# Performance work log

Hardware: AMD Instinct MI355X
Metric: run time of the kernel (lower is better)

The kernel has to match this reference:

```python
import jax, jax.numpy as jnp
import numpy as np

N = 50000   # n_nodes
E = 500000  # n_edges
D = 128     # input_dim == hidden_dim
L = 2       # n_layers
K = 5       # Chebyshev filter size


def setup_inputs() -> dict:
    key = jax.random.key(0)
    k0, k1, k2, k3, k4 = jax.random.split(key, 5)
    scale = 1.0 / np.sqrt(D)
    return {
        "edge_index": jax.random.randint(k0, (2, E), 0, N),
        "edge_weight": jax.random.uniform(k1, (E,), dtype=jnp.float32),
        "emb": jax.random.uniform(k2, (N, D), dtype=jnp.float32, minval=-1.0, maxval=1.0),
        "Wx": jax.random.normal(k3, (L, 3, K, D, D), dtype=jnp.float32) * scale,
        "bx": jnp.zeros((L, 3, D), dtype=jnp.float32),
        "Wh": jax.random.normal(k4, (L, 3, K, D, D), dtype=jnp.float32) * scale,
        "bh": jnp.zeros((L, 3, D), dtype=jnp.float32),
    }


def reference(edge_index, edge_weight, emb, Wx, bx, Wh, bh):
    src, dst = edge_index[0], edge_index[1]
    # ChebConv sym-normalized scaled Laplacian with lambda_max=2:
    # L_hat = L - I = -D^{-1/2} A D^{-1/2} (zero diagonal)
    deg = jax.ops.segment_sum(edge_weight, src, num_segments=N)
    dinv = jnp.where(deg > 0, deg ** -0.5, 0.0)
    w = -dinv[src] * edge_weight * dinv[dst]  # [E]

    def prop(x):  # L_hat @ x via gather/scatter over edges
        return jax.ops.segment_sum(w[:, None] * x[src], dst, num_segments=N)

    def cheb(x, W, b):  # sum_k T_k(L_hat) x W_k + b
        Tx0 = x
        out = Tx0 @ W[0]
        Tx1 = prop(Tx0)
        out = out + Tx1 @ W[1]
        for k in range(2, K):
            Tx2 = 2.0 * prop(Tx1) - Tx0
            out = out + Tx2 @ W[k]
            Tx0, Tx1 = Tx1, Tx2
        return out + b

    x = emb
    hidden_states = []
    for l in range(L):
        H = jnp.ones((N, D), x.dtype)  # init__hidd: ones
        Z = jax.nn.sigmoid(cheb(x, Wx[l, 0], bx[l, 0]) + cheb(H, Wh[l, 0], bh[l, 0]))
        R = jax.nn.sigmoid(cheb(x, Wx[l, 1], bx[l, 1]) + cheb(H, Wh[l, 1], bh[l, 1]))
        Ht = jnp.tanh(cheb(x, Wx[l, 2], bx[l, 2]) + cheb(H * R, Wh[l, 2], bh[l, 2]))
        Hn = Z * H + (1.0 - Z) * Ht
        h = jax.nn.relu(Hn)  # dropout is identity in eval mode
        hidden_states.append(h)
        x = h
    return x  # == hidden_states[-1]
```

## Files before the change

kernel.cpp:

```cpp
#include <hip/hip_runtime.h>
#include <math.h>

#define NN 50000
#define EE 500000
#define DD 128
#define KK 5
#define LL 2

typedef _Float16 f16x8 __attribute__((ext_vector_type(8)));
typedef float f32x4 __attribute__((ext_vector_type(4)));

__device__ __forceinline__ ushort f2h(float x) {
    union { _Float16 h; ushort u; } v; v.h = (_Float16)x; return v.u;
}


__global__ __launch_bounds__(256) void edge_pass1(
    const int* __restrict__ src, const int* __restrict__ dst,
    const float* __restrict__ ew,
    float* __restrict__ deg, int* __restrict__ hist)
{
    int e = blockIdx.x * blockDim.x + threadIdx.x;
    if (e >= EE) return;
    atomicAdd(&deg[src[e]], ew[e]);
    atomicAdd(&hist[dst[e]], 1);
}

__global__ __launch_bounds__(256) void dinv_kernel(
    const float* __restrict__ deg, float* __restrict__ dinv)
{
    int i = blockIdx.x * blockDim.x + threadIdx.x;
    if (i >= NN) return;
    float d = deg[i];
    dinv[i] = (d > 0.f) ? (1.f / sqrtf(d)) : 0.f;
}

#define SCAN_C ((NN + 1023) / 1024)
__global__ __launch_bounds__(1024) void scan_kernel(
    const int* __restrict__ hist, int* __restrict__ row_ptr)
{
    __shared__ int sums[1024];
    const int t = threadIdx.x;
    const int base = t * SCAN_C;
    int local[SCAN_C];
    int s = 0;
#pragma unroll
    for (int j = 0; j < SCAN_C; ++j) {
        int i = base + j;
        int v = (i < NN) ? hist[i] : 0;
        s += v;
        local[j] = s;
    }
    sums[t] = s;
    __syncthreads();
    for (int off = 1; off < 1024; off <<= 1) {
        int v = (t >= off) ? sums[t - off] : 0;
        __syncthreads();
        sums[t] += v;
        __syncthreads();
    }
    int excl = sums[t] - s;
    if (t == 0) row_ptr[0] = 0;
#pragma unroll
    for (int j = 0; j < SCAN_C; ++j) {
        int i = base + j;
        if (i < NN) row_ptr[i + 1] = excl + local[j];
    }
}

__global__ __launch_bounds__(256) void copy_fill(
    const int* __restrict__ row_ptr, int* __restrict__ fill)
{
    int i = blockIdx.x * blockDim.x + threadIdx.x;
    if (i < NN) fill[i] = row_ptr[i];
}

__global__ __launch_bounds__(256) void edge_scatter(
    const int* __restrict__ src, const int* __restrict__ dst,
    const float* __restrict__ ew, const float* __restrict__ dinv,
    int* __restrict__ fill,
    int* __restrict__ src_srt, float* __restrict__ w_srt)
{
    int e = blockIdx.x * blockDim.x + threadIdx.x;
    if (e >= EE) return;
    int s = src[e], t = dst[e];
    float w = -dinv[s] * ew[e] * dinv[t];
    int pos = atomicAdd(&fill[t], 1);
    src_srt[pos] = s;
    w_srt[pos] = w;
}

__global__ __launch_bounds__(256) void propv_kernel(
    const int* __restrict__ rp, const int* __restrict__ ss, const float* __restrict__ sw,
    const float* __restrict__ tin, const float* __restrict__ tprev, float* __restrict__ tout,
    float alpha, float beta, int ones_in, int ones_prev)
{
    int i = blockIdx.x * blockDim.x + threadIdx.x;
    if (i >= NN) return;
    float acc = 0.f;
    int e0 = rp[i], e1 = rp[i + 1];
    int e = e0;
    for (; e + 4 <= e1; e += 4) {
        float t0 = ones_in ? 1.f : tin[ss[e]];
        float t1v = ones_in ? 1.f : tin[ss[e + 1]];
        float t2v = ones_in ? 1.f : tin[ss[e + 2]];
        float t3v = ones_in ? 1.f : tin[ss[e + 3]];
        acc += sw[e] * t0 + sw[e + 1] * t1v + sw[e + 2] * t2v + sw[e + 3] * t3v;
    }
    for (; e < e1; ++e) {
        float tv = ones_in ? 1.f : tin[ss[e]];
        acc += sw[e] * tv;
    }
    float pv = ones_prev ? 1.f : (tprev ? tprev[i] : 0.f);
    tout[i] = alpha * acc + beta * pv;
}

__global__ __launch_bounds__(128) void colsum_kernel(
    const float* __restrict__ Wh, float* __restrict__ scol)
{
    int b = blockIdx.x;
    int k = b % KK;
    int g = (b / KK) % 2;
    int l = b / (2 * KK);
    int d = threadIdx.x;
    const float* Wp = Wh + ((size_t)((l * 3 + g) * KK + k)) * DD * DD;
    float s = 0.f;
    for (int r = 0; r < DD; ++r) s += Wp[r * DD + d];
    scol[((size_t)((l * 2 + g) * KK + k)) * DD + d] = s;
}

__global__ __launch_bounds__(256) void wconv_f16(
    const float* __restrict__ W, ushort* __restrict__ out, int mode)
{
    int t = blockIdx.x;
    int st = (mode == 0) ? t : ((t / KK) * 3 + 2) * KK + (t % KK);
    const float* Wp = W + (size_t)st * DD * DD;
    ushort* op = out + (size_t)t * DD * DD;
    for (int idx = threadIdx.x; idx < DD * DD; idx += 256) {
        int rb = idx >> 7, c = idx & 127;
        float w = Wp[c * DD + rb];
        int byte = rb * 256 + (((c * 2) ^ ((rb & 7) << 4)));
        *(ushort*)((char*)op + byte) = f2h(w);
    }
}

__global__ __launch_bounds__(256) void f32_to_f16(
    const float* __restrict__ in, ushort* __restrict__ out, int n8)
{
    int i = blockIdx.x * blockDim.x + threadIdx.x;
    if (i >= n8) return;
    float4 a = ((const float4*)in)[i * 2];
    float4 b = ((const float4*)in)[i * 2 + 1];
    f16x8 o;
    o[0] = (_Float16)a.x; o[1] = (_Float16)a.y; o[2] = (_Float16)a.z; o[3] = (_Float16)a.w;
    o[4] = (_Float16)b.x; o[5] = (_Float16)b.y; o[6] = (_Float16)b.z; o[7] = (_Float16)b.w;
    ((f16x8*)out)[i] = o;
}

__global__ __launch_bounds__(256) void prop_mat(
    const int* __restrict__ rp, const int* __restrict__ ss, const float* __restrict__ sw,
    const ushort* __restrict__ x, const ushort* __restrict__ prev,
    ushort* __restrict__ out, float alpha, float beta)
{
    int node = blockIdx.x * 16 + (threadIdx.x >> 4);
    if (node >= NN) return;
    int lane = threadIdx.x & 15;
    int c = lane * 8;
    float acc[8];
#pragma unroll
    for (int j = 0; j < 8; ++j) acc[j] = 0.f;
    int e0 = rp[node], e1 = rp[node + 1];
    int e = e0;
    for (; e + 4 <= e1; e += 4) {
        int s0 = ss[e], s1 = ss[e + 1], s2 = ss[e + 2], s3 = ss[e + 3];
        float w0 = sw[e], w1 = sw[e + 1], w2 = sw[e + 2], w3 = sw[e + 3];
        f16x8 r0 = *(const f16x8*)(x + (size_t)s0 * DD + c);
        f16x8 r1 = *(const f16x8*)(x + (size_t)s1 * DD + c);
        f16x8 r2 = *(const f16x8*)(x + (size_t)s2 * DD + c);
        f16x8 r3 = *(const f16x8*)(x + (size_t)s3 * DD + c);
#pragma unroll
        for (int j = 0; j < 8; ++j)
            acc[j] += w0 * (float)r0[j] + w1 * (float)r1[j] + w2 * (float)r2[j] + w3 * (float)r3[j];
    }
    for (; e < e1; ++e) {
        int s = ss[e];
        float w = sw[e];
        f16x8 r = *(const f16x8*)(x + (size_t)s * DD + c);
#pragma unroll
        for (int j = 0; j < 8; ++j) acc[j] += w * (float)r[j];
    }
    f16x8 o;
    if (beta != 0.f && prev) {
        f16x8 pv = *(const f16x8*)(prev + (size_t)node * DD + c);
#pragma unroll
        for (int j = 0; j < 8; ++j) o[j] = (_Float16)(alpha * acc[j] + beta * (float)pv[j]);
    } else {
#pragma unroll
        for (int j = 0; j < 8; ++j) o[j] = (_Float16)(alpha * acc[j]);
    }
    *(f16x8*)(out + (size_t)node * DD + c) = o;
}

__device__ __forceinline__ void mm_gate(
    const ushort* __restrict__ const* Ts, const ushort* __restrict__ Wg,
    ushort* Bs, int rowg0, int rowg1, bool ok0, bool ok1,
    int tid, int lk, f32x4 acc[2][8], int lr)
{
#pragma unroll
    for (int fr = 0; fr < 2; ++fr)
#pragma unroll
        for (int fc = 0; fc < 8; ++fc) acc[fr][fc] = (f32x4){0.f, 0.f, 0.f, 0.f};
#pragma unroll
    for (int k = 0; k < KK; ++k) {
        const ushort* Tk = Ts[k];
        const ushort* Bg = Wg + (size_t)k * (DD * DD);
        __syncthreads();
#pragma unroll
        for (int i = 0; i < 8; ++i) {
            int off = i * 4096 + tid * 16;
            uint4 v = *(const uint4*)((const char*)Bg + off);
            *(uint4*)((char*)Bs + off) = v;
        }
        f16x8 a[2][4];
#pragma unroll
        for (int fr = 0; fr < 2; ++fr) {
            int rowg = fr ? rowg1 : rowg0;
            bool ok = fr ? ok1 : ok0;
            const ushort* rp2 = Ts[k] + (size_t)rowg * DD + lk * 8;
            (void)Tk;
#pragma unroll
            for (int ko = 0; ko < 4; ++ko) {
                if (ok) a[fr][ko] = *(const f16x8*)(rp2 + ko * 32);
                else a[fr][ko] = (f16x8){0, 0, 0, 0, 0, 0, 0, 0};
            }
        }
        __syncthreads();
#pragma unroll
        for (int ko = 0; ko < 4; ++ko) {
            const int cb = ko * 64 + lk * 16;
#pragma unroll
            for (int fc = 0; fc < 8; ++fc) {
                int rb = fc * 16 + lr;
                int byte = (rb * 256 + cb) ^ ((rb & 7) << 4);
                f16x8 bfrag = *(const f16x8*)((const char*)Bs + byte);
                acc[0][fc] = __builtin_amdgcn_mfma_f32_16x16x32_f16(a[0][ko], bfrag, acc[0][fc], 0, 0, 0);
                acc[1][fc] = __builtin_amdgcn_mfma_f32_16x16x32_f16(a[1][ko], bfrag, acc[1][fc], 0, 0, 0);
            }
        }
    }
}

__device__ __forceinline__ int xcd_swz(int b, int nwg) {
    int xcd = b & 7, idx = b >> 3;
    int q = nwg >> 3, rr = nwg & 7;
    int start = (xcd < rr) ? xcd * (q + 1) : rr * (q + 1) + (xcd - rr) * q;
    return start + idx;
}

__global__ __launch_bounds__(256) void cheb_mm_zr(
    const ushort* __restrict__ T0, const ushort* __restrict__ T1,
    const ushort* __restrict__ T2, const ushort* __restrict__ T3,
    const ushort* __restrict__ T4,
    const ushort* __restrict__ Wt,
    const float* __restrict__ tvec, const float* __restrict__ scol,
    const float* __restrict__ bx, const float* __restrict__ bh, int l,
    float* __restrict__ Xz, ushort* __restrict__ Xr16, float* __restrict__ Xh)
{
    __shared__ ushort Bs[DD * DD];
    const int tile = xcd_swz(blockIdx.x, gridDim.x);
    const int tid = threadIdx.x;
    const int lane = tid & 63;
    const int wid = tid >> 6;
    const int lr = lane & 15;
    const int lk = lane >> 4;
    const int r0 = tile * 128;
    const ushort* Ts[5] = {T0, T1, T2, T3, T4};

    int rowg0 = r0 + wid * 32 + lr;
    int rowg1 = rowg0 + 16;
    bool ok0 = rowg0 < NN;
    bool ok1 = rowg1 < NN;

    f32x4 accZ[2][8], accB[2][8];
    mm_gate(Ts, Wt, Bs, rowg0, rowg1, ok0, ok1, tid, lk, accZ, lr);
    mm_gate(Ts, Wt + (size_t)KK * DD * DD, Bs, rowg0, rowg1, ok0, ok1, tid, lk, accB, lr);

    {
        const float* s0 = scol + (size_t)((l * 2 + 0) * KK) * DD;
        const float* s1 = scol + (size_t)((l * 2 + 1) * KK) * DD;
        const float* bz0 = bx + (size_t)(l * 3 + 0) * DD;
        const float* bz1 = bh + (size_t)(l * 3 + 0) * DD;
        const float* br0 = bx + (size_t)(l * 3 + 1) * DD;
        const float* br1 = bh + (size_t)(l * 3 + 1) * DD;
#pragma unroll
        for (int fr = 0; fr < 2; ++fr) {
#pragma unroll
            for (int j = 0; j < 4; ++j) {
                int grow = r0 + wid * 32 + fr * 16 + lk * 4 + j;
                if (grow < NN) {
                    float t1 = tvec[grow], t2 = tvec[NN + grow];
                    float t3 = tvec[2 * NN + grow], t4 = tvec[3 * NN + grow];
#pragma unroll
                    for (int fc = 0; fc < 8; ++fc) {
                        int d = fc * 16 + lr;
                        size_t idx = (size_t)grow * DD + d;
                        float hz = s0[d] + t1 * s0[DD + d] + t2 * s0[2 * DD + d]
                                 + t3 * s0[3 * DD + d] + t4 * s0[4 * DD + d];
                        float z = accZ[fr][fc][j] + bz0[d] + bz1[d] + hz;
                        z = 1.f / (1.f + expf(-z));
                        float hr = s1[d] + t1 * s1[DD + d] + t2 * s1[2 * DD + d]
                                 + t3 * s1[3 * DD + d] + t4 * s1[4 * DD + d];
                        float r = accB[fr][fc][j] + br0[d] + br1[d] + hr;
                        r = 1.f / (1.f + expf(-r));
                        Xz[idx] = z;
                        Xr16[idx] = f2h(r);
                    }
                }
            }
        }
    }

    mm_gate(Ts, Wt + (size_t)2 * KK * DD * DD, Bs, rowg0, rowg1, ok0, ok1, tid, lk, accZ, lr);
#pragma unroll
    for (int fr = 0; fr < 2; ++fr) {
#pragma unroll
        for (int j = 0; j < 4; ++j) {
            int grow = r0 + wid * 32 + fr * 16 + lk * 4 + j;
            if (grow < NN) {
#pragma unroll
                for (int fc = 0; fc < 8; ++fc) {
                    int d = fc * 16 + lr;
                    Xh[(size_t)grow * DD + d] = accZ[fr][fc][j];
                }
            }
        }
    }
}

__global__ __launch_bounds__(256) void cheb_mm_final(
    const ushort* __restrict__ T0, const ushort* __restrict__ T1,
    const ushort* __restrict__ T2, const ushort* __restrict__ T3,
    const ushort* __restrict__ T4,
    const ushort* __restrict__ Wt,
    const float* __restrict__ Xh, const float* __restrict__ Xz,
    const float* __restrict__ bx, const float* __restrict__ bh, int l,
    float* __restrict__ out, ushort* __restrict__ h16, int write_f32)
{
    __shared__ ushort Bs[DD * DD];
    const int tile = xcd_swz(blockIdx.x, gridDim.x);
    const int tid = threadIdx.x;
    const int lane = tid & 63;
    const int wid = tid >> 6;
    const int lr = lane & 15;
    const int lk = lane >> 4;
    const int r0 = tile * 128;
    const ushort* Ts[5] = {T0, T1, T2, T3, T4};

    int rowg0 = r0 + wid * 32 + lr;
    int rowg1 = rowg0 + 16;
    bool ok0 = rowg0 < NN;
    bool ok1 = rowg1 < NN;

    f32x4 acc[2][8];
    mm_gate(Ts, Wt, Bs, rowg0, rowg1, ok0, ok1, tid, lk, acc, lr);

    const float* b0 = bx + (size_t)(l * 3 + 2) * DD;
    const float* b1 = bh + (size_t)(l * 3 + 2) * DD;
#pragma unroll
    for (int fr = 0; fr < 2; ++fr) {
#pragma unroll
        for (int j = 0; j < 4; ++j) {
            int grow = r0 + wid * 32 + fr * 16 + lk * 4 + j;
            if (grow < NN) {
#pragma unroll
                for (int fc = 0; fc < 8; ++fc) {
                    int d = fc * 16 + lr;
                    size_t idx = (size_t)grow * DD + d;
                    float pre = acc[fr][fc][j] + Xh[idx] + b0[d] + b1[d];
                    float ht = tanhf(pre);
                    float z = Xz[idx];
                    float hn = z + (1.f - z) * ht;
                    float h = hn > 0.f ? hn : 0.f;
                    if (write_f32) out[idx] = h;
                    h16[idx] = f2h(h);
                }
            }
        }
    }
}


extern "C" void kernel_launch(void* const* d_in, const int* in_sizes, int n_in,
                              void* d_out, int out_size, void* d_ws, size_t ws_size,
                              hipStream_t stream)
{
    const int*   ei  = (const int*)d_in[0];
    const float* ew  = (const float*)d_in[1];
    const float* emb = (const float*)d_in[2];
    const float* Wx  = (const float*)d_in[3];
    const float* bx  = (const float*)d_in[4];
    const float* Wh  = (const float*)d_in[5];
    const float* bh  = (const float*)d_in[6];
    float* out = (float*)d_out;

    const int* src = ei;
    const int* dst = ei + EE;

    char* ws = (char*)d_ws;
    size_t off = 0;
    auto alloc = [&](size_t nbytes) -> char* {
        char* p = ws + off;
        off = (off + nbytes + 255) & ~(size_t)255;
        return p;
    };
    float*  deg     = (float*)alloc((size_t)NN * 4);
    float*  dinv    = (float*)alloc((size_t)NN * 4);
    int*    hist    = (int*)alloc((size_t)(NN + 1) * 4);
    int*    row_ptr = (int*)alloc((size_t)(NN + 1) * 4);
    int*    fill    = (int*)alloc((size_t)(NN + 1) * 4);
    int*    src_srt = (int*)alloc((size_t)EE * 4);
    float*  w_srt   = (float*)alloc((size_t)EE * 4);
    float*  tvec    = (float*)alloc((size_t)4 * NN * 4);
    float*  scol    = (float*)alloc((size_t)LL * 2 * KK * DD * 4);
    float*  Xz      = (float*)alloc((size_t)NN * DD * 4);
    float*  Xh      = (float*)alloc((size_t)NN * DD * 4);
    ushort* Th      = (ushort*)alloc((size_t)4 * NN * DD * 2);
    ushort* x_f16   = (ushort*)alloc((size_t)NN * DD * 2);
    ushort* Xr_f16  = (ushort*)alloc((size_t)NN * DD * 2);
    ushort* WxT     = (ushort*)alloc((size_t)LL * 3 * KK * DD * DD * 2);
    ushort* WhT2    = (ushort*)alloc((size_t)LL * KK * DD * DD * 2);
    (void)ws_size; (void)in_sizes; (void)n_in; (void)out_size;

    ushort* T1 = Th;
    ushort* T2 = Th + (size_t)NN * DD;
    ushort* T3 = Th + (size_t)2 * NN * DD;
    ushort* T4 = Th + (size_t)3 * NN * DD;

    const int EG = (EE + 255) / 256;
    const int NG = (NN + 255) / 256;
    const int PG = (NN + 15) / 16;
    const int MMG = (NN + 127) / 128;
    const int CVG = (NN * DD / 8 + 255) / 256;
    const int GATE_STRIDE = KK * DD * DD;

    hipMemsetAsync(deg, 0, (size_t)NN * 4, stream);
    hipMemsetAsync(hist, 0, (size_t)(NN + 1) * 4, stream);

    edge_pass1<<<EG, 256, 0, stream>>>(src, dst, ew, deg, hist);
    dinv_kernel<<<NG, 256, 0, stream>>>(deg, dinv);
    scan_kernel<<<1, 1024, 0, stream>>>(hist, row_ptr);
    copy_fill<<<NG, 256, 0, stream>>>(row_ptr, fill);
    edge_scatter<<<EG, 256, 0, stream>>>(src, dst, ew, dinv, fill, src_srt, w_srt);

    float* t1 = tvec;
    float* t2 = tvec + NN;
    float* t3 = tvec + 2 * NN;
    float* t4 = tvec + 3 * NN;
    propv_kernel<<<NG, 256, 0, stream>>>(row_ptr, src_srt, w_srt, nullptr, nullptr, t1, 1.f,  0.f, 1, 0);
    propv_kernel<<<NG, 256, 0, stream>>>(row_ptr, src_srt, w_srt, t1, nullptr,      t2, 2.f, -1.f, 0, 1);
    propv_kernel<<<NG, 256, 0, stream>>>(row_ptr, src_srt, w_srt, t2, t1,           t3, 2.f, -1.f, 0, 0);
    propv_kernel<<<NG, 256, 0, stream>>>(row_ptr, src_srt, w_srt, t3, t2,           t4, 2.f, -1.f, 0, 0);

    colsum_kernel<<<LL * 2 * KK, 128, 0, stream>>>(Wh, scol);

    wconv_f16<<<LL * 3 * KK, 256, 0, stream>>>(Wx, WxT, 0);
    wconv_f16<<<LL * KK, 256, 0, stream>>>(Wh, WhT2, 1);

    f32_to_f16<<<CVG, 256, 0, stream>>>(emb, x_f16, NN * DD / 8);

    for (int l = 0; l < LL; ++l) {
        prop_mat<<<PG, 256, 0, stream>>>(row_ptr, src_srt, w_srt, x_f16, nullptr, T1, 1.f,  0.f);
        prop_mat<<<PG, 256, 0, stream>>>(row_ptr, src_srt, w_srt, T1,    x_f16,   T2, 2.f, -1.f);
        prop_mat<<<PG, 256, 0, stream>>>(row_ptr, src_srt, w_srt, T2,    T1,      T3, 2.f, -1.f);
        prop_mat<<<PG, 256, 0, stream>>>(row_ptr, src_srt, w_srt, T3,    T2,      T4, 2.f, -1.f);

        cheb_mm_zr<<<MMG, 256, 0, stream>>>(x_f16, T1, T2, T3, T4,
                                            WxT + (size_t)l * 3 * GATE_STRIDE,
                                            tvec, scol, bx, bh, l,
                                            Xz, Xr_f16, Xh);

        prop_mat<<<PG, 256, 0, stream>>>(row_ptr, src_srt, w_srt, Xr_f16, nullptr, T1, 1.f,  0.f);
        prop_mat<<<PG, 256, 0, stream>>>(row_ptr, src_srt, w_srt, T1,     Xr_f16,  T2, 2.f, -1.f);
        prop_mat<<<PG, 256, 0, stream>>>(row_ptr, src_srt, w_srt, T2,     T1,      T3, 2.f, -1.f);
        prop_mat<<<PG, 256, 0, stream>>>(row_ptr, src_srt, w_srt, T3,     T2,      T4, 2.f, -1.f);

        cheb_mm_final<<<MMG, 256, 0, stream>>>(Xr_f16, T1, T2, T3, T4,
                                               WhT2 + (size_t)l * GATE_STRIDE,
                                               Xh, Xz, bx, bh, l,
                                               out, x_f16, (l == LL - 1) ? 1 : 0);
    }
}
```

Measured before the change: 957.5 us.

## Split gate matmuls across blocks and unroll SpMM edge loop by eight

The fused x-side Chebyshev matmul kernel, which computed all three gates sequentially per 128-row tile, is replaced by a generic kernel launched with three times as many blocks, one gate each. This writes raw fp32 gate outputs to a new buffer, and a separate elementwise kernel applies the sigmoid for Z and R. The aim is more parallelism and fewer live accumulators per block. The cost is an extra fp32 write and read of the R pre-activation plus a new kernel launch. Separately, the sparse propagation loop gains an 8-edge unrolled path to put more gathers in flight.

```diff
diff --git a/kernel.cpp b/kernel.cpp
--- a/kernel.cpp
+++ b/kernel.cpp
@@ -171,6 +171,24 @@
     for (int j = 0; j < 8; ++j) acc[j] = 0.f;
     int e0 = rp[node], e1 = rp[node + 1];
     int e = e0;
+    for (; e + 8 <= e1; e += 8) {
+        int s0 = ss[e], s1 = ss[e + 1], s2 = ss[e + 2], s3 = ss[e + 3];
+        int s4 = ss[e + 4], s5 = ss[e + 5], s6 = ss[e + 6], s7 = ss[e + 7];
+        float w0 = sw[e], w1 = sw[e + 1], w2 = sw[e + 2], w3 = sw[e + 3];
+        float w4 = sw[e + 4], w5 = sw[e + 5], w6 = sw[e + 6], w7 = sw[e + 7];
+        f16x8 r0 = *(const f16x8*)(x + (size_t)s0 * DD + c);
+        f16x8 r1 = *(const f16x8*)(x + (size_t)s1 * DD + c);
+        f16x8 r2 = *(const f16x8*)(x + (size_t)s2 * DD + c);
+        f16x8 r3 = *(const f16x8*)(x + (size_t)s3 * DD + c);
+        f16x8 r4 = *(const f16x8*)(x + (size_t)s4 * DD + c);
+        f16x8 r5 = *(const f16x8*)(x + (size_t)s5 * DD + c);
+        f16x8 r6 = *(const f16x8*)(x + (size_t)s6 * DD + c);
+        f16x8 r7 = *(const f16x8*)(x + (size_t)s7 * DD + c);
+#pragma unroll
+        for (int j = 0; j < 8; ++j)
+            acc[j] += w0 * (float)r0[j] + w1 * (float)r1[j] + w2 * (float)r2[j] + w3 * (float)r3[j]
+                    + w4 * (float)r4[j] + w5 * (float)r5[j] + w6 * (float)r6[j] + w7 * (float)r7[j];
+    }
     for (; e + 4 <= e1; e += 4) {
         int s0 = ss[e], s1 = ss[e + 1], s2 = ss[e + 2], s3 = ss[e + 3];
         float w0 = sw[e], w1 = sw[e + 1], w2 = sw[e + 2], w3 = sw[e + 3];
@@ -212,7 +230,6 @@
         for (int fc = 0; fc < 8; ++fc) acc[fr][fc] = (f32x4){0.f, 0.f, 0.f, 0.f};
 #pragma unroll
     for (int k = 0; k < KK; ++k) {
-        const ushort* Tk = Ts[k];
         const ushort* Bg = Wg + (size_t)k * (DD * DD);
         __syncthreads();
 #pragma unroll
@@ -227,7 +244,6 @@
             int rowg = fr ? rowg1 : rowg0;
             bool ok = fr ? ok1 : ok0;
             const ushort* rp2 = Ts[k] + (size_t)rowg * DD + lk * 8;
-            (void)Tk;
 #pragma unroll
             for (int ko = 0; ko < 4; ++ko) {
                 if (ok) a[fr][ko] = *(const f16x8*)(rp2 + ko * 32);
@@ -257,17 +273,18 @@
     return start + idx;
 }
 
-__global__ __launch_bounds__(256) void cheb_mm_zr(
+__global__ __launch_bounds__(256) void cheb_mm_mfma(
     const ushort* __restrict__ T0, const ushort* __restrict__ T1,
     const ushort* __restrict__ T2, const ushort* __restrict__ T3,
     const ushort* __restrict__ T4,
-    const ushort* __restrict__ Wt,
-    const float* __restrict__ tvec, const float* __restrict__ scol,
-    const float* __restrict__ bx, const float* __restrict__ bh, int l,
-    float* __restrict__ Xz, ushort* __restrict__ Xr16, float* __restrict__ Xh)
+    const ushort* __restrict__ Wt, int gate_stride,
+    float* __restrict__ outbase, size_t out_stride, int ngates)
 {
     __shared__ ushort Bs[DD * DD];
-    const int tile = xcd_swz(blockIdx.x, gridDim.x);
+    const int lin = xcd_swz(blockIdx.x, gridDim.x);
+    const int tile = lin / ngates;
+    const int g = lin - tile * ngates;
+
     const int tid = threadIdx.x;
     const int lane = tid & 63;
     const int wid = tid >> 6;
@@ -281,46 +298,10 @@
     bool ok0 = rowg0 < NN;
     bool ok1 = rowg1 < NN;
 
-    f32x4 accZ[2][8], accB[2][8];
-    mm_gate(Ts, Wt, Bs, rowg0, rowg1, ok0, ok1, tid, lk, accZ, lr);
-    mm_gate(Ts, Wt + (size_t)KK * DD * DD, Bs, rowg0, rowg1, ok0, ok1, tid, lk, accB, lr);
-
-    {
-        const float* s0 = scol + (size_t)((l * 2 + 0) * KK) * DD;
-        const float* s1 = scol + (size_t)((l * 2 + 1) * KK) * DD;
-        const float* bz0 = bx + (size_t)(l * 3 + 0) * DD;
-        const float* bz1 = bh + (size_t)(l * 3 + 0) * DD;
-        const float* br0 = bx + (size_t)(l * 3 + 1) * DD;
-        const float* br1 = bh + (size_t)(l * 3 + 1) * DD;
-#pragma unroll
-        for (int fr = 0; fr < 2; ++fr) {
-#pragma unroll
-            for (int j = 0; j < 4; ++j) {
-                int grow = r0 + wid * 32 + fr * 16 + lk * 4 + j;
-                if (grow < NN) {
-                    float t1 = tvec[grow], t2 = tvec[NN + grow];
-                    float t3 = tvec[2 * NN + grow], t4 = tvec[3 * NN + grow];
-#pragma unroll
-                    for (int fc = 0; fc < 8; ++fc) {
-                        int d = fc * 16 + lr;
-                        size_t idx = (size_t)grow * DD + d;
-                        float hz = s0[d] + t1 * s0[DD + d] + t2 * s0[2 * DD + d]
-                                 + t3 * s0[3 * DD + d] + t4 * s0[4 * DD + d];
-                        float z = accZ[fr][fc][j] + bz0[d] + bz1[d] + hz;
-                        z = 1.f / (1.f + expf(-z));
-                        float hr = s1[d] + t1 * s1[DD + d] + t2 * s1[2 * DD + d]
-                                 + t3 * s1[3 * DD + d] + t4 * s1[4 * DD + d];
-                        float r = accB[fr][fc][j] + br0[d] + br1[d] + hr;
-                        r = 1.f / (1.f + expf(-r));
-                        Xz[idx] = z;
-                        Xr16[idx] = f2h(r);
-                    }
-                }
-            }
-        }
-    }
-
-    mm_gate(Ts, Wt + (size_t)2 * KK * DD * DD, Bs, rowg0, rowg1, ok0, ok1, tid, lk, accZ, lr);
+    f32x4 acc[2][8];
+    mm_gate(Ts, Wt + (size_t)g * gate_stride, Bs, rowg0, rowg1, ok0, ok1, tid, lk, acc, lr);
+
+    float* outp = outbase + (size_t)g * out_stride;
 #pragma unroll
     for (int fr = 0; fr < 2; ++fr) {
 #pragma unroll
@@ -329,8 +310,8 @@
             if (grow < NN) {
 #pragma unroll
                 for (int fc = 0; fc < 8; ++fc) {
-                    int d = fc * 16 + lr;
-                    Xh[(size_t)grow * DD + d] = accZ[fr][fc][j];
+                    int col = fc * 16 + lr;
+                    outp[(size_t)grow * DD + col] = acc[fr][fc][j];
                 }
             }
         }
@@ -387,6 +368,28 @@
             }
         }
     }
+}
+
+__global__ __launch_bounds__(256) void gate_zr_kernel(
+    float* __restrict__ Xz, const float* __restrict__ Xr, ushort* __restrict__ Xr_f16,
+    const float* __restrict__ tvec, const float* __restrict__ scol,
+    const float* __restrict__ bx, const float* __restrict__ bh, int l)
+{
+    int idx = blockIdx.x * blockDim.x + threadIdx.x;
+    if (idx >= NN * DD) return;
+    int i = idx >> 7;
+    int d = idx & 127;
+    float t1 = tvec[i], t2 = tvec[NN + i], t3 = tvec[2 * NN + i], t4 = tvec[3 * NN + i];
+
+    const float* s0 = scol + (size_t)((l * 2 + 0) * KK) * DD;
+    float hz = s0[d] + t1 * s0[DD + d] + t2 * s0[2 * DD + d] + t3 * s0[3 * DD + d] + t4 * s0[4 * DD + d];
+    float z = Xz[idx] + bx[(l * 3 + 0) * DD + d] + bh[(l * 3 + 0) * DD + d] + hz;
+    Xz[idx] = 1.f / (1.f + expf(-z));
+
+    const float* s1 = scol + (size_t)((l * 2 + 1) * KK) * DD;
+    float hr = s1[d] + t1 * s1[DD + d] + t2 * s1[2 * DD + d] + t3 * s1[3 * DD + d] + t4 * s1[4 * DD + d];
+    float r = Xr[idx] + bx[(l * 3 + 1) * DD + d] + bh[(l * 3 + 1) * DD + d] + hr;
+    Xr_f16[idx] = f2h(1.f / (1.f + expf(-r)));
 }
 
 
@@ -422,8 +425,7 @@
     float*  w_srt   = (float*)alloc((size_t)EE * 4);
     float*  tvec    = (float*)alloc((size_t)4 * NN * 4);
     float*  scol    = (float*)alloc((size_t)LL * 2 * KK * DD * 4);
-    float*  Xz      = (float*)alloc((size_t)NN * DD * 4);
-    float*  Xh      = (float*)alloc((size_t)NN * DD * 4);
+    float*  X       = (float*)alloc((size_t)3 * NN * DD * 4);
     ushort* Th      = (ushort*)alloc((size_t)4 * NN * DD * 2);
     ushort* x_f16   = (ushort*)alloc((size_t)NN * DD * 2);
     ushort* Xr_f16  = (ushort*)alloc((size_t)NN * DD * 2);
@@ -431,6 +433,9 @@
     ushort* WhT2    = (ushort*)alloc((size_t)LL * KK * DD * DD * 2);
     (void)ws_size; (void)in_sizes; (void)n_in; (void)out_size;
 
+    float* Xz = X;
+    float* Xr = X + (size_t)NN * DD;
+    float* Xh = X + (size_t)2 * NN * DD;
     ushort* T1 = Th;
     ushort* T2 = Th + (size_t)NN * DD;
     ushort* T3 = Th + (size_t)2 * NN * DD;
@@ -439,6 +444,7 @@
     const int EG = (EE + 255) / 256;
     const int NG = (NN + 255) / 256;
     const int PG = (NN + 15) / 16;
+    const int ELG = (NN * DD + 255) / 256;
     const int MMG = (NN + 127) / 128;
     const int CVG = (NN * DD / 8 + 255) / 256;
     const int GATE_STRIDE = KK * DD * DD;
@@ -474,10 +480,11 @@
         prop_mat<<<PG, 256, 0, stream>>>(row_ptr, src_srt, w_srt, T2,    T1,      T3, 2.f, -1.f);
         prop_mat<<<PG, 256, 0, stream>>>(row_ptr, src_srt, w_srt, T3,    T2,      T4, 2.f, -1.f);
 
-        cheb_mm_zr<<<MMG, 256, 0, stream>>>(x_f16, T1, T2, T3, T4,
-                                            WxT + (size_t)l * 3 * GATE_STRIDE,
-                                            tvec, scol, bx, bh, l,
-                                            Xz, Xr_f16, Xh);
+        cheb_mm_mfma<<<MMG * 3, 256, 0, stream>>>(x_f16, T1, T2, T3, T4,
+                                             WxT + (size_t)l * 3 * GATE_STRIDE, GATE_STRIDE,
+                                             Xz, (size_t)NN * DD, 3);
+
+        gate_zr_kernel<<<ELG, 256, 0, stream>>>(Xz, Xr, Xr_f16, tvec, scol, bx, bh, l);
 
         prop_mat<<<PG, 256, 0, stream>>>(row_ptr, src_srt, w_srt, Xr_f16, nullptr, T1, 1.f,  0.f);
         prop_mat<<<PG, 256, 0, stream>>>(row_ptr, src_srt, w_srt, T1,     Xr_f16,  T2, 2.f, -1.f);
```

Result: faster. 863.9 us (-9.8%).
